# Optimization experiments

Measured on AMD Instinct MI355X. Metric: run time of the kernel, lower is better.

The kernel has to match this reference:

```python
import jax, jax.numpy as jnp
import numpy as np

HID = 16

def _lrconv(x, edge_index, edge_attr, w1, b1, w2, b2):
    # flow='target_to_source': x_i = x[edge_index[0]], x_j = x[edge_index[1]],
    # aggregate (max) at edge_index[0].
    src = edge_index[0]
    dst = edge_index[1]
    m = jnp.concatenate([x[src], x[dst], edge_attr], axis=-1)  # [E, 2*in+edge]
    m = jax.nn.relu(m @ w1 + b1)
    m = jax.nn.relu(m @ w2 + b2)  # [E, out], all >= 0
    agg = jax.ops.segment_max(m, src, num_segments=x.shape[0])
    # empty segments get -inf in jax; PyG fills with 0. Messages are ReLU'd (>=0),
    # so clamping at 0 is exact.
    return jnp.maximum(agg, 0.0)

def _glorot(key, shape):
    fan_in, fan_out = shape
    lim = float(np.sqrt(6.0 / (fan_in + fan_out)))
    return jax.random.uniform(key, shape, jnp.float32, -lim, lim)

def setup_inputs() -> dict:
    key = jax.random.key(0)
    ks = jax.random.split(key, 16)
    N, E = 100000, 1600000
    x = jax.random.normal(ks[0], (N, 4), jnp.float32)
    edge_index = jax.random.randint(ks[1], (2, E), 0, N, jnp.int64)
    edge_attr = jax.random.normal(ks[2], (E, 8), jnp.float32)
    # conv1: in=4 -> cat dim 4*2+8=16
    c1_w1 = _glorot(ks[3], (16, HID)); c1_b1 = jnp.zeros((HID,), jnp.float32)
    c1_w2 = _glorot(ks[4], (HID, 16)); c1_b2 = jnp.zeros((16,), jnp.float32)
    # conv2: in=16 -> cat dim 16*2+8=40
    c2_w1 = _glorot(ks[5], (40, HID)); c2_b1 = jnp.zeros((HID,), jnp.float32)
    c2_w2 = _glorot(ks[6], (HID, 16)); c2_b2 = jnp.zeros((16,), jnp.float32)
    l1_w = _glorot(ks[7], (16, 16)); l1_b = jnp.zeros((16,), jnp.float32)
    l2_w = _glorot(ks[8], (16, 1)); l2_b = jnp.zeros((1,), jnp.float32)
    return {"x": x, "edge_index": edge_index, "edge_attr": edge_attr,
            "c1_w1": c1_w1, "c1_b1": c1_b1, "c1_w2": c1_w2, "c1_b2": c1_b2,
            "c2_w1": c2_w1, "c2_b1": c2_b1, "c2_w2": c2_w2, "c2_b2": c2_b2,
            "l1_w": l1_w, "l1_b": l1_b, "l2_w": l2_w, "l2_b": l2_b}

def reference(x, edge_index, edge_attr,
              c1_w1, c1_b1, c1_w2, c1_b2,
              c2_w1, c2_b1, c2_w2, c2_b2,
              l1_w, l1_b, l2_w, l2_b):
    h = _lrconv(x, edge_index, edge_attr, c1_w1, c1_b1, c1_w2, c1_b2)   # [N,16]
    h = _lrconv(h, edge_index, edge_attr, c2_w1, c2_b1, c2_w2, c2_b2)   # [N,16]
    h = jax.nn.relu(h @ l1_w + l1_b)
    return h @ l2_w + l2_b  # [N,1]
```

## Files before the change

### kernel.cpp

```cpp
#include <hip/hip_runtime.h>
#include <hip/hip_fp16.h>

#define CHUNK 1024
#define NBKT 8

typedef _Float16 half8 __attribute__((ext_vector_type(8)));
typedef _Float16 half4 __attribute__((ext_vector_type(4)));
typedef float floatx4 __attribute__((ext_vector_type(4)));

union H8 { half8 h; unsigned int u[4]; };

__device__ __forceinline__ half8 hmax8(half8 a, half8 b) {
#if __has_builtin(__builtin_elementwise_max)
    return __builtin_elementwise_max(a, b);
#else
    half8 r;
    #pragma unroll
    for (int j = 0; j < 8; ++j) r[j] = a[j] > b[j] ? a[j] : b[j];
    return r;
#endif
}

__global__ __launch_bounds__(256) void rank_cvt(
    const int* __restrict__ ei, const float* __restrict__ ea,
    const float* __restrict__ x,
    int* __restrict__ deg, unsigned short* __restrict__ r,
    _Float16* __restrict__ eah, _Float16* __restrict__ xh,
    int E, int N)
{
    int e = blockIdx.x * 256 + threadIdx.x;
    if (e >= E) return;
    r[e] = (unsigned short)atomicAdd(&deg[(size_t)ei[e] * NBKT + ((e >> 8) & (NBKT - 1))], 1);
    float4 a0 = *(const float4*)(ea + (size_t)e * 8);
    float4 a1 = *(const float4*)(ea + (size_t)e * 8 + 4);
    half8 h;
    h[0] = (_Float16)a0.x; h[1] = (_Float16)a0.y;
    h[2] = (_Float16)a0.z; h[3] = (_Float16)a0.w;
    h[4] = (_Float16)a1.x; h[5] = (_Float16)a1.y;
    h[6] = (_Float16)a1.z; h[7] = (_Float16)a1.w;
    *(half8*)(eah + (size_t)e * 8) = h;
    if (e < N) {
        float4 xv = *(const float4*)(x + (size_t)e * 4);
        half4 hx;
        hx[0] = (_Float16)xv.x; hx[1] = (_Float16)xv.y;
        hx[2] = (_Float16)xv.z; hx[3] = (_Float16)xv.w;
        *(half4*)(xh + (size_t)e * 4) = hx;
    }
}

__global__ __launch_bounds__(256) void scan_chunk_sums(
    const int* __restrict__ v, int* __restrict__ csum, int N)
{
    __shared__ int s[256];
    int base = blockIdx.x * CHUNK;
    int t = threadIdx.x;
    int acc = 0;
    #pragma unroll
    for (int i = 0; i < CHUNK / 256; ++i) {
        int idx = base + t + i * 256;
        if (idx < N) acc += v[idx];
    }
    s[t] = acc; __syncthreads();
    for (int o = 128; o > 0; o >>= 1) {
        if (t < o) s[t] += s[t + o];
        __syncthreads();
    }
    if (t == 0) csum[blockIdx.x] = s[0];
}

__global__ __launch_bounds__(256) void scan_chunk_off(
    const int* __restrict__ csum, int* __restrict__ coff, int nch)
{
    __shared__ int s[256];
    __shared__ int carry;
    int t = threadIdx.x;
    if (t == 0) carry = 0;
    __syncthreads();
    for (int base = 0; base < nch; base += 256) {
        int v = (base + t < nch) ? csum[base + t] : 0;
        s[t] = v; __syncthreads();
        for (int o = 1; o < 256; o <<= 1) {
            int add = (t >= o) ? s[t - o] : 0;
            __syncthreads();
            s[t] += add;
            __syncthreads();
        }
        int excl = carry + (t > 0 ? s[t - 1] : 0);
        if (base + t < nch) coff[base + t] = excl;
        __syncthreads();
        if (t == 0) carry += s[255];
        __syncthreads();
    }
}

__global__ __launch_bounds__(256) void scan_within_excl(
    const int* __restrict__ deg, int* __restrict__ pos,
    const int* __restrict__ coff, int N)
{
    __shared__ int s[256];
    int t = threadIdx.x;
    int base = blockIdx.x * CHUNK + t * 4;
    int v0 = 0, v1 = 0, v2 = 0, v3 = 0;
    if (base + 0 < N) v0 = deg[base + 0];
    if (base + 1 < N) v1 = deg[base + 1];
    if (base + 2 < N) v2 = deg[base + 2];
    if (base + 3 < N) v3 = deg[base + 3];
    s[t] = v0 + v1 + v2 + v3;
    __syncthreads();
    for (int o = 1; o < 256; o <<= 1) {
        int add = (t >= o) ? s[t - o] : 0;
        __syncthreads();
        s[t] += add;
        __syncthreads();
    }
    int run = coff[blockIdx.x] + (t > 0 ? s[t - 1] : 0);
    if (base + 0 < N) pos[base + 0] = run; run += v0;
    if (base + 1 < N) pos[base + 1] = run; run += v1;
    if (base + 2 < N) pos[base + 2] = run; run += v2;
    if (base + 3 < N) pos[base + 3] = run;
}

__global__ __launch_bounds__(256) void edge_mlp1(
    const _Float16* __restrict__ xh,
    const int*   __restrict__ ei,
    const _Float16* __restrict__ eah,
    const int*   __restrict__ pos,
    const unsigned short* __restrict__ r,
    const float* __restrict__ w1, const float* __restrict__ b1,
    const float* __restrict__ w2, const float* __restrict__ b2,
    _Float16* __restrict__ m2h,
    int E)
{
    __shared__ _Float16 itm[4][8][16][24];
    int tid = threadIdx.x;
    int w = tid >> 6, lane = tid & 63;
    int e16 = lane & 15, q = lane >> 4;
    int ebase = (blockIdx.x * 4 + w) << 7;
    if (ebase >= E) return;
    int e0 = ebase + lane;
    int e1 = ebase + 64 + lane;

    int s0 = 0, d0 = 0, p0 = 0, s1 = 0, d1 = 0, p1 = 0;
    if (e0 < E) {
        s0 = ei[e0]; d0 = ei[E + e0];
        p0 = pos[(size_t)s0 * NBKT + ((e0 >> 8) & (NBKT - 1))] + (int)r[e0];
    }
    if (e1 < E) {
        s1 = ei[e1]; d1 = ei[E + e1];
        p1 = pos[(size_t)s1 * NBKT + ((e1 >> 8) & (NBKT - 1))] + (int)r[e1];
    }

    half8 B1, B2;
    #pragma unroll
    for (int j = 0; j < 8; ++j) { B1[j] = (_Float16)0.f; B2[j] = (_Float16)0.f; }
    if (q < 2) {
        #pragma unroll
        for (int j = 0; j < 8; ++j) {
            B1[j] = (_Float16)w1[(8 * q + j) * 16 + e16];
            B2[j] = (_Float16)w2[(8 * q + j) * 16 + e16];
        }
    }
    float b1c = b1[e16], b2c = b2[e16];

    half8 A[8];
    #pragma unroll
    for (int t = 0; t < 8; ++t) {
        int tt = t & 3;
        int st = (t < 4) ? __shfl(s0, 16 * tt + e16, 64) : __shfl(s1, 16 * tt + e16, 64);
        int dt = (t < 4) ? __shfl(d0, 16 * tt + e16, 64) : __shfl(d1, 16 * tt + e16, 64);
        half8 a;
        #pragma unroll
        for (int j = 0; j < 8; ++j) a[j] = (_Float16)0.f;
        int et = ebase + 16 * t + e16;
        if (q == 0 && et < E) {
            half4 hs = *(const half4*)(xh + (size_t)st * 4);
            half4 hd = *(const half4*)(xh + (size_t)dt * 4);
            a[0] = hs[0]; a[1] = hs[1]; a[2] = hs[2]; a[3] = hs[3];
            a[4] = hd[0]; a[5] = hd[1]; a[6] = hd[2]; a[7] = hd[3];
        } else if (q == 1 && et < E) {
            a = *(const half8*)(eah + (size_t)et * 8);
        }
        A[t] = a;
    }

    floatx4 C[8];
    #pragma unroll
    for (int t = 0; t < 8; ++t) {
        floatx4 c = {b1c, b1c, b1c, b1c};
        C[t] = __builtin_amdgcn_mfma_f32_16x16x32_f16(A[t], B1, c, 0, 0, 0);
    }
    #pragma unroll
    for (int t = 0; t < 8; ++t)
        #pragma unroll
        for (int i = 0; i < 4; ++i)
            itm[w][t][4 * q + i][e16] = (_Float16)fmaxf(C[t][i], 0.0f);
    __builtin_amdgcn_wave_barrier();

    half8 A2[8];
    #pragma unroll
    for (int t = 0; t < 8; ++t) {
        half8 a;
        #pragma unroll
        for (int j = 0; j < 8; ++j) a[j] = (_Float16)0.f;
        if (q < 2) a = *(const half8*)&itm[w][t][e16][8 * q];
        A2[t] = a;
    }
    __builtin_amdgcn_wave_barrier();
    floatx4 C2[8];
    #pragma unroll
    for (int t = 0; t < 8; ++t) {
        floatx4 c = {b2c, b2c, b2c, b2c};
        C2[t] = __builtin_amdgcn_mfma_f32_16x16x32_f16(A2[t], B2, c, 0, 0, 0);
    }
    #pragma unroll
    for (int t = 0; t < 8; ++t)
        #pragma unroll
        for (int i = 0; i < 4; ++i)
            itm[w][t][4 * q + i][e16] = (_Float16)C2[t][i];
    __builtin_amdgcn_wave_barrier();

    if (e0 < E) {
        half8 lo = *(const half8*)&itm[w][q][e16][0];
        half8 hi = *(const half8*)&itm[w][q][e16][8];
        *(half8*)(m2h + (size_t)p0 * 16)     = lo;
        *(half8*)(m2h + (size_t)p0 * 16 + 8) = hi;
    }
    if (e1 < E) {
        half8 lo = *(const half8*)&itm[w][q + 4][e16][0];
        half8 hi = *(const half8*)&itm[w][q + 4][e16][8];
        *(half8*)(m2h + (size_t)p1 * 16)     = lo;
        *(half8*)(m2h + (size_t)p1 * 16 + 8) = hi;
    }
}

__global__ __launch_bounds__(256) void edge_mlp2(
    const _Float16* __restrict__ h1,
    const int*   __restrict__ ei,
    const _Float16* __restrict__ eah,
    const int*   __restrict__ pos,
    const unsigned short* __restrict__ r,
    const float* __restrict__ w1, const float* __restrict__ b1v,
    const float* __restrict__ w2, const float* __restrict__ b2,
    _Float16* __restrict__ m2h, int E)
{
    __shared__ _Float16 itm[4][8][16][24];
    int tid = threadIdx.x;
    int w = tid >> 6, lane = tid & 63;
    int e16 = lane & 15, q = lane >> 4;
    int ebase = (blockIdx.x * 4 + w) << 7;
    if (ebase >= E) return;
    int e0 = ebase + lane;
    int e1 = ebase + 64 + lane;

    int s0 = 0, d0 = 0, p0 = 0, s1 = 0, d1 = 0, p1 = 0;
    if (e0 < E) {
        s0 = ei[e0]; d0 = ei[E + e0];
        p0 = pos[(size_t)s0 * NBKT + ((e0 >> 8) & (NBKT - 1))] + (int)r[e0];
    }
    if (e1 < E) {
        s1 = ei[e1]; d1 = ei[E + e1];
        p1 = pos[(size_t)s1 * NBKT + ((e1 >> 8) & (NBKT - 1))] + (int)r[e1];
    }

    half8 B1, B2e, BL2;
    #pragma unroll
    for (int j = 0; j < 8; ++j) {
        B1[j] = (_Float16)w1[(8 * q + j) * 16 + e16];
        B2e[j] = (_Float16)0.f; BL2[j] = (_Float16)0.f;
    }
    if (q == 0) {
        #pragma unroll
        for (int j = 0; j < 8; ++j)
            B2e[j] = (_Float16)w1[(32 + j) * 16 + e16];
    }
    if (q < 2) {
        #pragma unroll
        for (int j = 0; j < 8; ++j)
            BL2[j] = (_Float16)w2[(8 * q + j) * 16 + e16];
    }
    float b1c = b1v[e16], b2c = b2[e16];

    half8 A1[8];
    #pragma unroll
    for (int t = 0; t < 8; ++t) {
        int tt = t & 3;
        int st = (t < 4) ? __shfl(s0, 16 * tt + e16, 64) : __shfl(s1, 16 * tt + e16, 64);
        int dt = (t < 4) ? __shfl(d0, 16 * tt + e16, 64) : __shfl(d1, 16 * tt + e16, 64);
        int row = (q < 2) ? st : dt;
        A1[t] = *(const half8*)(h1 + (size_t)row * 16 + 8 * (q & 1));
    }

    floatx4 C[8];
    #pragma unroll
    for (int t = 0; t < 8; ++t) {
        half8 a2;
        #pragma unroll
        for (int j = 0; j < 8; ++j) a2[j] = (_Float16)0.f;
        int et = ebase + 16 * t + e16;
        if (q == 0 && et < E)
            a2 = *(const half8*)(eah + (size_t)et * 8);
        floatx4 c = {b1c, b1c, b1c, b1c};
        c = __builtin_amdgcn_mfma_f32_16x16x32_f16(a2, B2e, c, 0, 0, 0);
        C[t] = __builtin_amdgcn_mfma_f32_16x16x32_f16(A1[t], B1, c, 0, 0, 0);
    }
    #pragma unroll
    for (int t = 0; t < 8; ++t)
        #pragma unroll
        for (int i = 0; i < 4; ++i)
            itm[w][t][4 * q + i][e16] = (_Float16)fmaxf(C[t][i], 0.0f);
    __builtin_amdgcn_wave_barrier();

    half8 A2L[8];
    #pragma unroll
    for (int t = 0; t < 8; ++t) {
        half8 a;
        #pragma unroll
        for (int j = 0; j < 8; ++j) a[j] = (_Float16)0.f;
        if (q < 2) a = *(const half8*)&itm[w][t][e16][8 * q];
        A2L[t] = a;
    }
    __builtin_amdgcn_wave_barrier();
    floatx4 C2[8];
    #pragma unroll
    for (int t = 0; t < 8; ++t) {
        floatx4 c = {b2c, b2c, b2c, b2c};
        C2[t] = __builtin_amdgcn_mfma_f32_16x16x32_f16(A2L[t], BL2, c, 0, 0, 0);
    }
    #pragma unroll
    for (int t = 0; t < 8; ++t)
        #pragma unroll
        for (int i = 0; i < 4; ++i)
            itm[w][t][4 * q + i][e16] = (_Float16)C2[t][i];
    __builtin_amdgcn_wave_barrier();

    if (e0 < E) {
        half8 lo = *(const half8*)&itm[w][q][e16][0];
        half8 hi = *(const half8*)&itm[w][q][e16][8];
        *(half8*)(m2h + (size_t)p0 * 16)     = lo;
        *(half8*)(m2h + (size_t)p0 * 16 + 8) = hi;
    }
    if (e1 < E) {
        half8 lo = *(const half8*)&itm[w][q + 4][e16][0];
        half8 hi = *(const half8*)&itm[w][q + 4][e16][8];
        *(half8*)(m2h + (size_t)p1 * 16)     = lo;
        *(half8*)(m2h + (size_t)p1 * 16 + 8) = hi;
    }
}

__global__ __launch_bounds__(256) void segmax1_h(
    const _Float16* __restrict__ m2h, const int* __restrict__ pos,
    unsigned int* __restrict__ h1u,
    int N, int E)
{
    int tid = threadIdx.x;
    int n = blockIdx.x * 32 + (tid >> 3);
    if (n >= N) return;
    int g = tid & 7;
    int start = pos[(size_t)n * NBKT];
    int end = (n + 1 < N) ? pos[(size_t)(n + 1) * NBKT] : E;

    half8 a0, a1;
    #pragma unroll
    for (int j = 0; j < 8; ++j) { a0[j] = (_Float16)0.f; a1[j] = (_Float16)0.f; }

    for (int k = start + g; k < end; k += 8) {
        half8 v0 = *(const half8*)(m2h + (size_t)k * 16);
        half8 v1 = *(const half8*)(m2h + (size_t)k * 16 + 8);
        a0 = hmax8(a0, v0);
        a1 = hmax8(a1, v1);
    }
    #pragma unroll
    for (int mask = 1; mask < 8; mask <<= 1) {
        H8 x0, x1, y0, y1;
        x0.h = a0; x1.h = a1;
        #pragma unroll
        for (int j = 0; j < 4; ++j) {
            y0.u[j] = __shfl_xor(x0.u[j], mask, 64);
            y1.u[j] = __shfl_xor(x1.u[j], mask, 64);
        }
        a0 = hmax8(a0, y0.h);
        a1 = hmax8(a1, y1.h);
    }
    H8 U0, U1; U0.h = a0; U1.h = a1;
    unsigned int word = (g < 4) ? U0.u[g & 3] : U1.u[g & 3];
    h1u[(size_t)n * 8 + g] = word;
}

__global__ __launch_bounds__(256) void segmax2_head(
    const _Float16* __restrict__ m2h, const int* __restrict__ pos,
    const float* __restrict__ l1w, const float* __restrict__ l1b,
    const float* __restrict__ l2w, const float* __restrict__ l2b,
    float* __restrict__ out, int N, int E)
{
    int tid = threadIdx.x;
    int n = blockIdx.x * 32 + (tid >> 3);
    if (n >= N) return;
    int g = tid & 7;
    int start = pos[(size_t)n * NBKT];
    int end = (n + 1 < N) ? pos[(size_t)(n + 1) * NBKT] : E;

    half8 a0, a1;
    #pragma unroll
    for (int j = 0; j < 8; ++j) { a0[j] = (_Float16)0.f; a1[j] = (_Float16)0.f; }

    for (int k = start + g; k < end; k += 8) {
        half8 v0 = *(const half8*)(m2h + (size_t)k * 16);
        half8 v1 = *(const half8*)(m2h + (size_t)k * 16 + 8);
        a0 = hmax8(a0, v0);
        a1 = hmax8(a1, v1);
    }
    #pragma unroll
    for (int mask = 1; mask < 8; mask <<= 1) {
        H8 x0, x1, y0, y1;
        x0.h = a0; x1.h = a1;
        #pragma unroll
        for (int j = 0; j < 4; ++j) {
            y0.u[j] = __shfl_xor(x0.u[j], mask, 64);
            y1.u[j] = __shfl_xor(x1.u[j], mask, 64);
        }
        a0 = hmax8(a0, y0.h);
        a1 = hmax8(a1, y1.h);
    }

    float acc[16];
    #pragma unroll
    for (int j = 0; j < 8; ++j) { acc[j] = (float)a0[j]; acc[8 + j] = (float)a1[j]; }

    float t2[16];
    #pragma unroll
    for (int j = 0; j < 16; ++j) t2[j] = l1b[j];
    #pragma unroll
    for (int kk = 0; kk < 16; ++kk) {
        float ak = acc[kk];
        #pragma unroll
        for (int j = 0; j < 16; ++j) t2[j] = fmaf(ak, l1w[kk * 16 + j], t2[j]);
    }
    float r2 = l2b[0];
    #pragma unroll
    for (int j = 0; j < 16; ++j) r2 = fmaf(fmaxf(t2[j], 0.0f), l2w[j], r2);
    if (g == 0) out[n] = r2;
}

extern "C" void kernel_launch(void* const* d_in, const int* in_sizes, int n_in,
                              void* d_out, int out_size, void* d_ws, size_t ws_size,
                              hipStream_t stream)
{
    const float* x     = (const float*)d_in[0];
    const int*   ei    = (const int*)  d_in[1];
    const float* ea    = (const float*)d_in[2];
    const float* c1_w1 = (const float*)d_in[3];
    const float* c1_b1 = (const float*)d_in[4];
    const float* c1_w2 = (const float*)d_in[5];
    const float* c1_b2 = (const float*)d_in[6];
    const float* c2_w1 = (const float*)d_in[7];
    const float* c2_b1 = (const float*)d_in[8];
    const float* c2_w2 = (const float*)d_in[9];
    const float* c2_b2 = (const float*)d_in[10];
    const float* l1_w  = (const float*)d_in[11];
    const float* l1_b  = (const float*)d_in[12];
    const float* l2_w  = (const float*)d_in[13];
    const float* l2_b  = (const float*)d_in[14];
    float* out = (float*)d_out;

    const int N = in_sizes[0] / 4;
    const int E = in_sizes[2] / 8;
    const int M = N * NBKT;
    const int nch = (M + CHUNK - 1) / CHUNK;

    const int BLK = 256;
    const int egrid = (E + BLK - 1) / BLK;
    const int ggrid = (N + 31) / 32;
    const int mgrid = (E + 511) / 512;

    size_t szPos = ((size_t)M * 4 + 15) & ~(size_t)15;
    size_t szR   = ((size_t)E * 2 + 15) & ~(size_t)15;
    size_t szXh  = ((size_t)N * 8 + 15) & ~(size_t)15;
    size_t szH1  = ((size_t)N * 32 + 15) & ~(size_t)15;
    size_t szEah = (size_t)E * 16;
    size_t szM2h = (size_t)E * 32;

    size_t pos_off = 0;
    size_t r_off   = pos_off + szPos;
    size_t xh_off  = r_off   + szR;
    size_t h1_off  = xh_off  + szXh;
    size_t eah_off = h1_off  + szH1;
    size_t m2h_off = eah_off + szEah;
    size_t deg_off = m2h_off;
    size_t cs_off  = deg_off + szPos;
    size_t cf_off  = cs_off + 16384;

    int*            pos  = (int*)  ((char*)d_ws + pos_off);
    unsigned short* r    = (unsigned short*)((char*)d_ws + r_off);
    _Float16*       xh   = (_Float16*)((char*)d_ws + xh_off);
    _Float16*       h1   = (_Float16*)((char*)d_ws + h1_off);
    _Float16*       eah  = (_Float16*)((char*)d_ws + eah_off);
    _Float16*       m2h  = (_Float16*)((char*)d_ws + m2h_off);
    int*            deg  = (int*)  ((char*)d_ws + deg_off);
    int*            csum = (int*)  ((char*)d_ws + cs_off);
    int*            coff = (int*)  ((char*)d_ws + cf_off);

    hipMemsetAsync(deg, 0, (size_t)M * 4, stream);
    rank_cvt<<<egrid, BLK, 0, stream>>>(ei, ea, x, deg, r, eah, xh, E, N);
    scan_chunk_sums<<<nch, BLK, 0, stream>>>(deg, csum, M);
    scan_chunk_off<<<1, 256, 0, stream>>>(csum, coff, nch);
    scan_within_excl<<<nch, BLK, 0, stream>>>(deg, pos, coff, M);
    edge_mlp1<<<mgrid, BLK, 0, stream>>>(xh, ei, eah, pos, r,
                                         c1_w1, c1_b1, c1_w2, c1_b2, m2h, E);
    segmax1_h<<<ggrid, BLK, 0, stream>>>(m2h, pos, (unsigned int*)h1, N, E);
    edge_mlp2<<<mgrid, BLK, 0, stream>>>(h1, ei, eah, pos, r,
                                         c2_w1, c2_b1, c2_w2, c2_b2, m2h, E);
    segmax2_head<<<ggrid, BLK, 0, stream>>>(m2h, pos, l1_w, l1_b, l2_w, l2_b,
                                            out, N, E);
}
```

Measured before the change: 348.2 us.

## Pre-sort edges into CSR-ordered records so MLP kernels read and write contiguously

Adds a scatter kernel that writes each edge's (src, dst, fp16 attributes) into a 24-byte record at its CSR position. Both edge MLP kernels then walk edges in sorted order, so the message stores to m2h become contiguous instead of scattered, and the x[src] gathers gain locality. The 8-bucket degree split used to spread atomic contention is dropped in favour of a plain per-node counter, which shrinks the scan. In exchange there is an extra pass over all edges, and same-node atomics may contend more.

```diff
diff --git a/kernel.cpp b/kernel.cpp
--- a/kernel.cpp
+++ b/kernel.cpp
@@ -2,7 +2,7 @@
 #include <hip/hip_fp16.h>
 
 #define CHUNK 1024
-#define NBKT 8
+#define RECB 24
 
 typedef _Float16 half8 __attribute__((ext_vector_type(8)));
 typedef _Float16 half4 __attribute__((ext_vector_type(4)));
@@ -21,24 +21,27 @@
 #endif
 }
 
+__device__ __forceinline__ unsigned int pack2f(float a, float b) {
+    __half2 h = __floats2half2_rn(a, b);
+    return *(unsigned int*)&h;
+}
+
+__device__ __forceinline__ half8 load_attr(const char* __restrict__ rec, int et) {
+    union { unsigned int u[4]; half8 h; } cv;
+    uint2 lo = *(const uint2*)(rec + (size_t)et * RECB + 8);
+    uint2 hi = *(const uint2*)(rec + (size_t)et * RECB + 16);
+    cv.u[0] = lo.x; cv.u[1] = lo.y; cv.u[2] = hi.x; cv.u[3] = hi.y;
+    return cv.h;
+}
+
 __global__ __launch_bounds__(256) void rank_cvt(
-    const int* __restrict__ ei, const float* __restrict__ ea,
-    const float* __restrict__ x,
+    const int* __restrict__ ei, const float* __restrict__ x,
     int* __restrict__ deg, unsigned short* __restrict__ r,
-    _Float16* __restrict__ eah, _Float16* __restrict__ xh,
-    int E, int N)
+    _Float16* __restrict__ xh, int E, int N)
 {
     int e = blockIdx.x * 256 + threadIdx.x;
     if (e >= E) return;
-    r[e] = (unsigned short)atomicAdd(&deg[(size_t)ei[e] * NBKT + ((e >> 8) & (NBKT - 1))], 1);
-    float4 a0 = *(const float4*)(ea + (size_t)e * 8);
-    float4 a1 = *(const float4*)(ea + (size_t)e * 8 + 4);
-    half8 h;
-    h[0] = (_Float16)a0.x; h[1] = (_Float16)a0.y;
-    h[2] = (_Float16)a0.z; h[3] = (_Float16)a0.w;
-    h[4] = (_Float16)a1.x; h[5] = (_Float16)a1.y;
-    h[6] = (_Float16)a1.z; h[7] = (_Float16)a1.w;
-    *(half8*)(eah + (size_t)e * 8) = h;
+    r[e] = (unsigned short)atomicAdd(&deg[ei[e]], 1);
     if (e < N) {
         float4 xv = *(const float4*)(x + (size_t)e * 4);
         half4 hx;
@@ -120,12 +123,29 @@
     if (base + 3 < N) pos[base + 3] = run;
 }
 
+__global__ __launch_bounds__(256) void scatter_rec(
+    const int* __restrict__ ei, const float* __restrict__ ea,
+    const int* __restrict__ pos, const unsigned short* __restrict__ r,
+    char* __restrict__ rec, int E)
+{
+    int e = blockIdx.x * 256 + threadIdx.x;
+    if (e >= E) return;
+    int s = ei[e];
+    int d = ei[E + e];
+    int p = pos[s] + (int)r[e];
+    float4 a0 = *(const float4*)(ea + (size_t)e * 8);
+    float4 a1 = *(const float4*)(ea + (size_t)e * 8 + 4);
+    unsigned int h0 = pack2f(a0.x, a0.y), h1 = pack2f(a0.z, a0.w);
+    unsigned int h2 = pack2f(a1.x, a1.y), h3 = pack2f(a1.z, a1.w);
+    char* b = rec + (size_t)p * RECB;
+    *(int2*)b         = make_int2(s, d);
+    *(uint2*)(b + 8)  = make_uint2(h0, h1);
+    *(uint2*)(b + 16) = make_uint2(h2, h3);
+}
+
 __global__ __launch_bounds__(256) void edge_mlp1(
     const _Float16* __restrict__ xh,
-    const int*   __restrict__ ei,
-    const _Float16* __restrict__ eah,
-    const int*   __restrict__ pos,
-    const unsigned short* __restrict__ r,
+    const char*  __restrict__ rec,
     const float* __restrict__ w1, const float* __restrict__ b1,
     const float* __restrict__ w2, const float* __restrict__ b2,
     _Float16* __restrict__ m2h,
@@ -140,15 +160,9 @@
     int e0 = ebase + lane;
     int e1 = ebase + 64 + lane;
 
-    int s0 = 0, d0 = 0, p0 = 0, s1 = 0, d1 = 0, p1 = 0;
-    if (e0 < E) {
-        s0 = ei[e0]; d0 = ei[E + e0];
-        p0 = pos[(size_t)s0 * NBKT + ((e0 >> 8) & (NBKT - 1))] + (int)r[e0];
-    }
-    if (e1 < E) {
-        s1 = ei[e1]; d1 = ei[E + e1];
-        p1 = pos[(size_t)s1 * NBKT + ((e1 >> 8) & (NBKT - 1))] + (int)r[e1];
-    }
+    int s0 = 0, d0 = 0, s1 = 0, d1 = 0;
+    if (e0 < E) { int2 p = *(const int2*)(rec + (size_t)e0 * RECB); s0 = p.x; d0 = p.y; }
+    if (e1 < E) { int2 p = *(const int2*)(rec + (size_t)e1 * RECB); s1 = p.x; d1 = p.y; }
 
     half8 B1, B2;
     #pragma unroll
@@ -178,7 +192,7 @@
             a[0] = hs[0]; a[1] = hs[1]; a[2] = hs[2]; a[3] = hs[3];
             a[4] = hd[0]; a[5] = hd[1]; a[6] = hd[2]; a[7] = hd[3];
         } else if (q == 1 && et < E) {
-            a = *(const half8*)(eah + (size_t)et * 8);
+            a = load_attr(rec, et);
         }
         A[t] = a;
     }
@@ -222,23 +236,20 @@
     if (e0 < E) {
         half8 lo = *(const half8*)&itm[w][q][e16][0];
         half8 hi = *(const half8*)&itm[w][q][e16][8];
-        *(half8*)(m2h + (size_t)p0 * 16)     = lo;
-        *(half8*)(m2h + (size_t)p0 * 16 + 8) = hi;
+        *(half8*)(m2h + (size_t)e0 * 16)     = lo;
+        *(half8*)(m2h + (size_t)e0 * 16 + 8) = hi;
     }
     if (e1 < E) {
         half8 lo = *(const half8*)&itm[w][q + 4][e16][0];
         half8 hi = *(const half8*)&itm[w][q + 4][e16][8];
-        *(half8*)(m2h + (size_t)p1 * 16)     = lo;
-        *(half8*)(m2h + (size_t)p1 * 16 + 8) = hi;
+        *(half8*)(m2h + (size_t)e1 * 16)     = lo;
+        *(half8*)(m2h + (size_t)e1 * 16 + 8) = hi;
     }
 }
 
 __global__ __launch_bounds__(256) void edge_mlp2(
     const _Float16* __restrict__ h1,
-    const int*   __restrict__ ei,
-    const _Float16* __restrict__ eah,
-    const int*   __restrict__ pos,
-    const unsigned short* __restrict__ r,
+    const char*  __restrict__ rec,
     const float* __restrict__ w1, const float* __restrict__ b1v,
     const float* __restrict__ w2, const float* __restrict__ b2,
     _Float16* __restrict__ m2h, int E)
@@ -252,15 +263,9 @@
     int e0 = ebase + lane;
     int e1 = ebase + 64 + lane;
 
-    int s0 = 0, d0 = 0, p0 = 0, s1 = 0, d1 = 0, p1 = 0;
-    if (e0 < E) {
-        s0 = ei[e0]; d0 = ei[E + e0];
-        p0 = pos[(size_t)s0 * NBKT + ((e0 >> 8) & (NBKT - 1))] + (int)r[e0];
-    }
-    if (e1 < E) {
-        s1 = ei[e1]; d1 = ei[E + e1];
-        p1 = pos[(size_t)s1 * NBKT + ((e1 >> 8) & (NBKT - 1))] + (int)r[e1];
-    }
+    int s0 = 0, d0 = 0, s1 = 0, d1 = 0;
+    if (e0 < E) { int2 p = *(const int2*)(rec + (size_t)e0 * RECB); s0 = p.x; d0 = p.y; }
+    if (e1 < E) { int2 p = *(const int2*)(rec + (size_t)e1 * RECB); s1 = p.x; d1 = p.y; }
 
     half8 B1, B2e, BL2;
     #pragma unroll
@@ -298,7 +303,7 @@
         for (int j = 0; j < 8; ++j) a2[j] = (_Float16)0.f;
         int et = ebase + 16 * t + e16;
         if (q == 0 && et < E)
-            a2 = *(const half8*)(eah + (size_t)et * 8);
+            a2 = load_attr(rec, et);
         floatx4 c = {b1c, b1c, b1c, b1c};
         c = __builtin_amdgcn_mfma_f32_16x16x32_f16(a2, B2e, c, 0, 0, 0);
         C[t] = __builtin_amdgcn_mfma_f32_16x16x32_f16(A1[t], B1, c, 0, 0, 0);
@@ -336,14 +341,14 @@
     if (e0 < E) {
         half8 lo = *(const half8*)&itm[w][q][e16][0];
         half8 hi = *(const half8*)&itm[w][q][e16][8];
-        *(half8*)(m2h + (size_t)p0 * 16)     = lo;
-        *(half8*)(m2h + (size_t)p0 * 16 + 8) = hi;
+        *(half8*)(m2h + (size_t)e0 * 16)     = lo;
+        *(half8*)(m2h + (size_t)e0 * 16 + 8) = hi;
     }
     if (e1 < E) {
         half8 lo = *(const half8*)&itm[w][q + 4][e16][0];
         half8 hi = *(const half8*)&itm[w][q + 4][e16][8];
-        *(half8*)(m2h + (size_t)p1 * 16)     = lo;
-        *(half8*)(m2h + (size_t)p1 * 16 + 8) = hi;
+        *(half8*)(m2h + (size_t)e1 * 16)     = lo;
+        *(half8*)(m2h + (size_t)e1 * 16 + 8) = hi;
     }
 }
 
@@ -356,8 +361,8 @@
     int n = blockIdx.x * 32 + (tid >> 3);
     if (n >= N) return;
     int g = tid & 7;
-    int start = pos[(size_t)n * NBKT];
-    int end = (n + 1 < N) ? pos[(size_t)(n + 1) * NBKT] : E;
+    int start = pos[n];
+    int end = (n + 1 < N) ? pos[n + 1] : E;
 
     half8 a0, a1;
     #pragma unroll
@@ -396,8 +401,8 @@
     int n = blockIdx.x * 32 + (tid >> 3);
     if (n >= N) return;
     int g = tid & 7;
-    int start = pos[(size_t)n * NBKT];
-    int end = (n + 1 < N) ? pos[(size_t)(n + 1) * NBKT] : E;
+    int start = pos[n];
+    int end = (n + 1 < N) ? pos[n + 1] : E;
 
     half8 a0, a1;
     #pragma unroll
@@ -464,50 +469,50 @@
 
     const int N = in_sizes[0] / 4;
     const int E = in_sizes[2] / 8;
-    const int M = N * NBKT;
-    const int nch = (M + CHUNK - 1) / CHUNK;
+    const int nch = (N + CHUNK - 1) / CHUNK;
 
     const int BLK = 256;
     const int egrid = (E + BLK - 1) / BLK;
     const int ggrid = (N + 31) / 32;
     const int mgrid = (E + 511) / 512;
 
-    size_t szPos = ((size_t)M * 4 + 15) & ~(size_t)15;
+    size_t szPos = ((size_t)N * 4 + 15) & ~(size_t)15;
     size_t szR   = ((size_t)E * 2 + 15) & ~(size_t)15;
     size_t szXh  = ((size_t)N * 8 + 15) & ~(size_t)15;
     size_t szH1  = ((size_t)N * 32 + 15) & ~(size_t)15;
-    size_t szEah = (size_t)E * 16;
+    size_t szRec = ((size_t)E * RECB + 15) & ~(size_t)15;
     size_t szM2h = (size_t)E * 32;
 
     size_t pos_off = 0;
     size_t r_off   = pos_off + szPos;
     size_t xh_off  = r_off   + szR;
     size_t h1_off  = xh_off  + szXh;
-    size_t eah_off = h1_off  + szH1;
-    size_t m2h_off = eah_off + szEah;
+    size_t rec_off = h1_off  + szH1;
+    size_t m2h_off = rec_off + szRec;
     size_t deg_off = m2h_off;
     size_t cs_off  = deg_off + szPos;
-    size_t cf_off  = cs_off + 16384;
+    size_t cf_off  = cs_off + 4096;
 
     int*            pos  = (int*)  ((char*)d_ws + pos_off);
     unsigned short* r    = (unsigned short*)((char*)d_ws + r_off);
     _Float16*       xh   = (_Float16*)((char*)d_ws + xh_off);
     _Float16*       h1   = (_Float16*)((char*)d_ws + h1_off);
-    _Float16*       eah  = (_Float16*)((char*)d_ws + eah_off);
+    char*           rec  = (char*) ((char*)d_ws + rec_off);
     _Float16*       m2h  = (_Float16*)((char*)d_ws + m2h_off);
     int*            deg  = (int*)  ((char*)d_ws + deg_off);
     int*            csum = (int*)  ((char*)d_ws + cs_off);
     int*            coff = (int*)  ((char*)d_ws + cf_off);
 
-    hipMemsetAsync(deg, 0, (size_t)M * 4, stream);
-    rank_cvt<<<egrid, BLK, 0, stream>>>(ei, ea, x, deg, r, eah, xh, E, N);
-    scan_chunk_sums<<<nch, BLK, 0, stream>>>(deg, csum, M);
+    hipMemsetAsync(deg, 0, (size_t)N * 4, stream);
+    rank_cvt<<<egrid, BLK, 0, stream>>>(ei, x, deg, r, xh, E, N);
+    scan_chunk_sums<<<nch, BLK, 0, stream>>>(deg, csum, N);
     scan_chunk_off<<<1, 256, 0, stream>>>(csum, coff, nch);
-    scan_within_excl<<<nch, BLK, 0, stream>>>(deg, pos, coff, M);
-    edge_mlp1<<<mgrid, BLK, 0, stream>>>(xh, ei, eah, pos, r,
+    scan_within_excl<<<nch, BLK, 0, stream>>>(deg, pos, coff, N);
+    scatter_rec<<<egrid, BLK, 0, stream>>>(ei, ea, pos, r, rec, E);
+    edge_mlp1<<<mgrid, BLK, 0, stream>>>(xh, rec,
                                          c1_w1, c1_b1, c1_w2, c1_b2, m2h, E);
     segmax1_h<<<ggrid, BLK, 0, stream>>>(m2h, pos, (unsigned int*)h1, N, E);
-    edge_mlp2<<<mgrid, BLK, 0, stream>>>(h1, ei, eah, pos, r,
+    edge_mlp2<<<mgrid, BLK, 0, stream>>>(h1, rec,
                                          c2_w1, c2_b1, c2_w2, c2_b2, m2h, E);
     segmax2_head<<<ggrid, BLK, 0, stream>>>(m2h, pos, l1_w, l1_b, l2_w, l2_b,
                                             out, N, E);
```

Result: no change. 345.6 us (-0.7%).
